# Kernel tuning notes

Measured on AMD Instinct MI355X. Metric: run time of the kernel, lower is better.

The kernel has to match this reference:

```python
import jax, jax.numpy as jnp
import numpy as np

N = 50000
E = 500000
D_IN = 128
D_HID = 128  # hidden_channels; conv1 outputs 2*D_HID


def setup_inputs() -> dict:
    key = jax.random.key(0)
    ks = jax.random.split(key, 8)
    x = jax.random.normal(ks[0], (N, D_IN), dtype=jnp.float32)
    edge_index = jax.random.randint(ks[1], (2, E), 0, N, dtype=jnp.int64)
    # Glorot-ish init for weights, zeros for biases (PyG GCNConv default style)
    W1 = jax.random.normal(ks[2], (D_IN, 2 * D_HID), dtype=jnp.float32) / np.sqrt(D_IN)
    b1 = jnp.zeros((2 * D_HID,), dtype=jnp.float32)
    W2 = jax.random.normal(ks[3], (2 * D_HID, D_HID), dtype=jnp.float32) / np.sqrt(2 * D_HID)
    b2 = jnp.zeros((D_HID,), dtype=jnp.float32)
    Wfc = jax.random.normal(ks[4], (D_HID, 6), dtype=jnp.float32) / np.sqrt(D_HID)
    bfc = jnp.zeros((6,), dtype=jnp.float32)
    return {"x": x, "W1": W1, "b1": b1, "W2": W2, "b2": b2,
            "Wfc": Wfc, "bfc": bfc, "edge_index": edge_index}


def _gcn_conv(x, W, b, src, dst, deg_isqrt, n):
    # PyG GCNConv: h = W x; out_i = sum_j norm_ij * h_j + b, with self-loops
    h = x @ W                                  # [n, d_out]
    norm = deg_isqrt[src] * deg_isqrt[dst]     # [E+n]
    msg = h[src] * norm[:, None]               # gather + scale
    out = jax.ops.segment_sum(msg, dst, num_segments=n)  # scatter-add
    return out + b


def reference(x, W1, b1, W2, b2, Wfc, bfc, edge_index):
    n = x.shape[0]
    loop = jnp.arange(n, dtype=edge_index.dtype)
    src = jnp.concatenate([edge_index[0], loop])  # add self-loops
    dst = jnp.concatenate([edge_index[1], loop])
    deg = jax.ops.segment_sum(jnp.ones_like(dst, dtype=x.dtype), dst, num_segments=n)
    deg_isqrt = jnp.where(deg > 0, jax.lax.rsqrt(jnp.maximum(deg, 1e-12)), 0.0)
    h = jax.nn.relu(_gcn_conv(x, W1, b1, src, dst, deg_isqrt, n))
    h = jax.nn.relu(_gcn_conv(h, W2, b2, src, dst, deg_isqrt, n))
    return h @ Wfc + bfc
```

## Files before the change

kernel.cpp:

```cpp
#include <hip/hip_runtime.h>


typedef _Float16 f16;
typedef __attribute__((ext_vector_type(8))) _Float16 f16x8;
typedef __attribute__((ext_vector_type(4))) float f32x4;

__global__ void count_kernel(const int* __restrict__ dst, int* __restrict__ cnt,
                             int e) {
    for (int i = blockIdx.x * blockDim.x + threadIdx.x; i < e;
         i += gridDim.x * blockDim.x)
        atomicAdd(&cnt[dst[i]], 1);
}

__global__ void scan1_kernel(const int* __restrict__ cnt, int* __restrict__ local,
                             int* __restrict__ partials, float* __restrict__ disq,
                             int n) {
    __shared__ int lds[256];
    int base = blockIdx.x * 1024;
    int t = threadIdx.x;
    int v[4];
    int sum = 0;
    #pragma unroll
    for (int j = 0; j < 4; j++) {
        int i = base + t * 4 + j;
        v[j] = (i < n) ? cnt[i] : 0;
        if (i < n) disq[i] = rsqrtf(1.0f + (float)v[j]);
        sum += v[j];
    }
    lds[t] = sum;
    __syncthreads();
    for (int off = 1; off < 256; off <<= 1) {
        int x = (t >= off) ? lds[t - off] : 0;
        __syncthreads();
        lds[t] += x;
        __syncthreads();
    }
    int excl = lds[t] - sum;
    if (t == 255) partials[blockIdx.x] = lds[255];
    int run = excl;
    #pragma unroll
    for (int j = 0; j < 4; j++) {
        int i = base + t * 4 + j;
        if (i < n) local[i] = run;
        run += v[j];
    }
}

__global__ void scan2_kernel(int* __restrict__ partials, int nb) {
    __shared__ int lds[1024];
    int t = threadIdx.x;
    int v = (t < nb) ? partials[t] : 0;
    lds[t] = v;
    __syncthreads();
    for (int off = 1; off < 1024; off <<= 1) {
        int x = (t >= off) ? lds[t - off] : 0;
        __syncthreads();
        lds[t] += x;
        __syncthreads();
    }
    if (t < nb) partials[t] = lds[t] - v;
}

__global__ void scan3_kernel(const int* __restrict__ local,
                             const int* __restrict__ partials,
                             int* __restrict__ row_ptr, int* __restrict__ cursor,
                             int n, int e_total) {
    int base = blockIdx.x * 1024;
    int add = partials[blockIdx.x];
    int t = threadIdx.x;
    #pragma unroll
    for (int j = 0; j < 4; j++) {
        int i = base + t * 4 + j;
        if (i < n) {
            int p = local[i] + add;
            row_ptr[i] = p;
            cursor[i] = p;
        }
    }
    if (blockIdx.x == 0 && t == 0) row_ptr[n] = e_total;
}

__global__ void csr_fill_kernel(const int* __restrict__ src, const int* __restrict__ dst,
                                int* __restrict__ cursor, int* __restrict__ esorted,
                                int e) {
    for (int i = blockIdx.x * blockDim.x + threadIdx.x; i < e;
         i += gridDim.x * blockDim.x) {
        int d = dst[i];
        int pos = atomicAdd(&cursor[d], 1);
        esorted[pos] = src[i];
    }
}

__global__ void scale_cvt_kernel(const float4* __restrict__ in,
                                 const float* __restrict__ disq,
                                 f16* __restrict__ out, long long n4) {
    long long i = blockIdx.x * (long long)blockDim.x + threadIdx.x;
    if (i >= n4) return;
    float4 v = in[i];
    float s = disq[i >> 5];
    union { f16 h[4]; short4 s4; } u;
    u.h[0] = (f16)(v.x * s); u.h[1] = (f16)(v.y * s);
    u.h[2] = (f16)(v.z * s); u.h[3] = (f16)(v.w * s);
    *(short4*)(out + i * 4) = u.s4;
}

__global__ void cvt_wt_kernel(const float* __restrict__ W, f16* __restrict__ Wt,
                              int K, int Nc) {
    int i = blockIdx.x * blockDim.x + threadIdx.x;
    if (i >= K * Nc) return;
    int n = i / K, k = i - n * K;
    Wt[i] = (f16)W[(long long)k * Nc + n];
}

template <int MODE>
__global__ __launch_bounds__(256)
void gemm_f16_kernel(const f16* __restrict__ A,
                     const f16* __restrict__ Bt,
                     f16* __restrict__ C,
                     const float* __restrict__ rowscale,
                     const float* __restrict__ bias,
                     int M, int K, int Nc) {
    __shared__ __align__(16) char smem[(128 * 64 + 64 * 64) * 2];
    char* As = smem;
    char* Bs = smem + 128 * 64 * 2;
    const int tid = threadIdx.x;
    const int lane = tid & 63;
    const int wid = tid >> 6;
    const int wr = wid >> 1;
    const int wc = wid & 1;
    const int row0 = blockIdx.y * 128;
    const int col0 = blockIdx.x * 64;

    f32x4 acc[4][2];
    #pragma unroll
    for (int mr = 0; mr < 4; mr++)
        #pragma unroll
        for (int nr = 0; nr < 2; nr++)
            acc[mr][nr] = (f32x4){0.f, 0.f, 0.f, 0.f};

    for (int k0 = 0; k0 < K; k0 += 64) {
        #pragma unroll
        for (int i = 0; i < 4; i++) {
            int flat = tid + i * 256;
            int r = flat >> 3, g = flat & 7;
            int gr = row0 + r;
            float4 v = {0.f, 0.f, 0.f, 0.f};
            if (gr < M) v = *(const float4*)(A + (long long)gr * K + k0 + g * 8);
            *(float4*)(As + r * 128 + ((g * 16) ^ ((r & 7) << 4))) = v;
        }
        #pragma unroll
        for (int i = 0; i < 2; i++) {
            int flat = tid + i * 256;
            int nn = flat >> 3, g = flat & 7;
            float4 v = *(const float4*)(Bt + (long long)(col0 + nn) * K + k0 + g * 8);
            *(float4*)(Bs + nn * 128 + ((g * 16) ^ ((nn & 7) << 4))) = v;
        }
        __syncthreads();
        #pragma unroll
        for (int ks = 0; ks < 2; ks++) {
            const int kb = (ks * 32 + ((lane >> 4) * 8)) * 2;
            f16x8 af[4], bf[2];
            #pragma unroll
            for (int mr = 0; mr < 4; mr++) {
                int r = wr * 64 + mr * 16 + (lane & 15);
                af[mr] = *(const f16x8*)(As + r * 128 + (kb ^ ((r & 7) << 4)));
            }
            #pragma unroll
            for (int nr = 0; nr < 2; nr++) {
                int c = wc * 32 + nr * 16 + (lane & 15);
                bf[nr] = *(const f16x8*)(Bs + c * 128 + (kb ^ ((c & 7) << 4)));
            }
            #pragma unroll
            for (int mr = 0; mr < 4; mr++)
                #pragma unroll
                for (int nr = 0; nr < 2; nr++)
                    acc[mr][nr] = __builtin_amdgcn_mfma_f32_16x16x32_f16(
                        af[mr], bf[nr], acc[mr][nr], 0, 0, 0);
        }
        __syncthreads();
    }
    float bv[2] = {0.f, 0.f};
    if (MODE == 1) {
        #pragma unroll
        for (int nr = 0; nr < 2; nr++)
            bv[nr] = bias[col0 + wc * 32 + nr * 16 + (lane & 15)];
    }
    #pragma unroll
    for (int mr = 0; mr < 4; mr++) {
        #pragma unroll
        for (int reg = 0; reg < 4; reg++) {
            int row = row0 + wr * 64 + mr * 16 + (lane >> 4) * 4 + reg;
            if (row < M) {
                float s = rowscale[row];
                int col = col0 + wc * 32 + (lane & 15);
                #pragma unroll
                for (int nr = 0; nr < 2; nr++) {
                    float v = acc[mr][nr][reg] * s;
                    if (MODE == 1) v = fmaxf(v + bv[nr], 0.0f);
                    C[(long long)row * Nc + col + nr * 16] = (f16)v;
                }
            }
        }
    }
}

__global__ void gather_sum_f16_kernel(const float4* __restrict__ h,
                                      float4* __restrict__ out,
                                      const int* __restrict__ row_ptr,
                                      const int* __restrict__ esorted,
                                      int n, int c8) {
    int lane = threadIdx.x & 63;
    long long wave = (blockIdx.x * (long long)blockDim.x + threadIdx.x) >> 6;
    int epw = 64 / c8;
    int sub = lane / c8;
    int sl = lane - sub * c8;
    long long node = wave * epw + sub;
    if (node >= n) return;
    int beg = row_ptr[node], end = row_ptr[node + 1];
    float acc[8];
    {
        float4 v = h[node * c8 + sl];
        const f16* hp = (const f16*)&v;
        #pragma unroll
        for (int j = 0; j < 8; j++) acc[j] = (float)hp[j];
    }
    for (int e = beg; e < end; e++) {
        int s = esorted[e];
        float4 v = h[(long long)s * c8 + sl];
        const f16* hp = (const f16*)&v;
        #pragma unroll
        for (int j = 0; j < 8; j++) acc[j] += (float)hp[j];
    }
    union { float4 f4; f16 hh[8]; } o;
    #pragma unroll
    for (int j = 0; j < 8; j++) o.hh[j] = (f16)acc[j];
    out[node * c8 + sl] = o.f4;
}

__global__ void gather_fc_kernel(const float4* __restrict__ t,
                                 const int* __restrict__ row_ptr,
                                 const int* __restrict__ esorted,
                                 const float* __restrict__ disq,
                                 const float* __restrict__ b2,
                                 const float* __restrict__ Wfc,
                                 const float* __restrict__ bfc,
                                 float* __restrict__ out, int n) {
    __shared__ float wf[6 * 132];
    for (int i = threadIdx.x; i < 6 * 128; i += 256) {
        int k = i >> 7, ch = i & 127;
        wf[k * 132 + ch] = Wfc[ch * 6 + k];
    }
    __syncthreads();
    int lane = threadIdx.x & 63;
    long long wave = (blockIdx.x * (long long)blockDim.x + threadIdx.x) >> 6;
    int sub = lane >> 4;
    int sl = lane & 15;
    long long node = wave * 4 + sub;
    if (node >= n) return;
    int beg = row_ptr[node], end = row_ptr[node + 1];
    float acc[8];
    {
        float4 v = t[node * 16 + sl];
        const f16* hp = (const f16*)&v;
        #pragma unroll
        for (int j = 0; j < 8; j++) acc[j] = (float)hp[j];
    }
    for (int e = beg; e < end; e++) {
        int s = esorted[e];
        float4 v = t[(long long)s * 16 + sl];
        const f16* hp = (const f16*)&v;
        #pragma unroll
        for (int j = 0; j < 8; j++) acc[j] += (float)hp[j];
    }
    float sc = disq[node];
    const float4* b4 = (const float4*)(b2 + sl * 8);
    float4 bb0 = b4[0], bb1 = b4[1];
    float bb[8] = {bb0.x, bb0.y, bb0.z, bb0.w, bb1.x, bb1.y, bb1.z, bb1.w};
    float h2[8];
    #pragma unroll
    for (int j = 0; j < 8; j++)
        h2[j] = fmaxf(fmaf(acc[j], sc, bb[j]), 0.0f);
    float p[6];
    #pragma unroll
    for (int k = 0; k < 6; k++) {
        float s = 0.f;
        #pragma unroll
        for (int j = 0; j < 8; j++) s += h2[j] * wf[k * 132 + sl * 8 + j];
        p[k] = s;
    }
    #pragma unroll
    for (int off = 8; off >= 1; off >>= 1)
        #pragma unroll
        for (int k = 0; k < 6; k++) p[k] += __shfl_down(p[k], off);
    if (sl == 0) {
        #pragma unroll
        for (int k = 0; k < 6; k++)
            out[(long long)node * 6 + k] = p[k] + bfc[k];
    }
}

extern "C" void kernel_launch(void* const* d_in, const int* in_sizes, int n_in,
                              void* d_out, int out_size, void* d_ws, size_t ws_size,
                              hipStream_t stream) {
    const float* x   = (const float*)d_in[0];
    const float* W1  = (const float*)d_in[1];
    const float* b1  = (const float*)d_in[2];
    const float* W2  = (const float*)d_in[3];
    const float* b2  = (const float*)d_in[4];
    const float* Wfc = (const float*)d_in[5];
    const float* bfc = (const float*)d_in[6];
    const int* edges = (const int*)d_in[7];

    const int N = in_sizes[0] / 128;
    const int E = in_sizes[7] / 2;
    const int* e_src = edges;
    const int* e_dst = edges + E;

    char* ws = (char*)d_ws;
    size_t off = 0;
    auto alloc = [&](size_t bytes) {
        void* p = ws + off;
        off += (bytes + 255) & ~(size_t)255;
        return p;
    };
    const int NB = (N + 1023) / 1024;
    float* disq     = (float*)alloc((size_t)N * 4);
    int*   cnt      = (int*)  alloc((size_t)N * 4);
    int*   slocal   = (int*)  alloc((size_t)N * 4);
    int*   partials = (int*)  alloc((size_t)NB * 4);
    int*   row_ptr  = (int*)  alloc((size_t)(N + 1) * 4);
    int*   cursor   = (int*)  alloc((size_t)N * 4);
    int*   esorted  = (int*)  alloc((size_t)E * 4);
    f16*   xs       = (f16*)  alloc((size_t)N * 128 * 2);
    f16*   wt1      = (f16*)  alloc((size_t)256 * 128 * 2);
    f16*   wt2      = (f16*)  alloc((size_t)128 * 256 * 2);
    f16*   agg1     = (f16*)  alloc((size_t)N * 128 * 2);
    f16*   h1       = (f16*)  alloc((size_t)N * 256 * 2);
    f16*   tbuf     = (f16*)  alloc((size_t)N * 128 * 2);
    (void)ws_size; (void)n_in;

    float* out = (float*)d_out; (void)out_size;

    hipMemsetAsync(cnt, 0, (size_t)N * sizeof(int), stream);
    count_kernel<<<2048, 256, 0, stream>>>(e_dst, cnt, E);
    scan1_kernel<<<NB, 256, 0, stream>>>(cnt, slocal, partials, disq, N);
    scan2_kernel<<<1, 1024, 0, stream>>>(partials, NB);
    scan3_kernel<<<NB, 256, 0, stream>>>(slocal, partials, row_ptr, cursor, N, E);
    csr_fill_kernel<<<2048, 256, 0, stream>>>(e_src, e_dst, cursor, esorted, E);

    {
        long long n4 = (long long)N * 128 / 4;
        scale_cvt_kernel<<<(int)((n4 + 255) / 256), 256, 0, stream>>>(
            (const float4*)x, disq, xs, n4);
    }
    cvt_wt_kernel<<<(128 * 256 + 255) / 256, 256, 0, stream>>>(W1, wt1, 128, 256);
    cvt_wt_kernel<<<(256 * 128 + 255) / 256, 256, 0, stream>>>(W2, wt2, 256, 128);

    {
        long long waves = ((long long)N + 3) / 4;
        int blocks = (int)((waves + 3) / 4);
        gather_sum_f16_kernel<<<blocks, 256, 0, stream>>>(
            (const float4*)xs, (float4*)agg1, row_ptr, esorted, N, 16);
    }
    {
        dim3 g(256 / 64, (N + 127) / 128);
        gemm_f16_kernel<1><<<g, 256, 0, stream>>>(agg1, wt1, h1, disq, b1,
                                                  N, 128, 256);
    }

    {
        dim3 g(128 / 64, (N + 127) / 128);
        gemm_f16_kernel<0><<<g, 256, 0, stream>>>(h1, wt2, tbuf, disq, nullptr,
                                                  N, 256, 128);
    }
    {
        long long waves = ((long long)N + 3) / 4;
        int blocks = (int)((waves + 3) / 4);
        gather_fc_kernel<<<blocks, 256, 0, stream>>>(
            (const float4*)tbuf, row_ptr, esorted, disq, b2, Wfc, bfc, out, N);
    }
}
```

Measured before the change: 240.2 us.

## Double-buffer GEMM with direct global-to-LDS loads, unroll gathers, merge convert kernels

The GEMM now double-buffers LDS tiles and uses global_load_lds to fetch A and B tiles directly into pre-swizzled shared memory, overlapping loads for the next K-tile with MFMA compute. Partial row tiles fall back to a register path. The two gather kernels unroll the neighbor loop by four so more independent loads are in flight, and the input and weight conversion kernels are merged into one launch. The aim is to hide memory latency and cut launch overhead, at the cost of doubled LDS usage per block, which may lower occupancy.

```diff
diff --git a/kernel.cpp b/kernel.cpp
--- a/kernel.cpp
+++ b/kernel.cpp
@@ -4,6 +4,11 @@
 typedef _Float16 f16;
 typedef __attribute__((ext_vector_type(8))) _Float16 f16x8;
 typedef __attribute__((ext_vector_type(4))) float f32x4;
+
+#define GLOAD16(g, l)                                                      \
+    __builtin_amdgcn_global_load_lds(                                      \
+        (const __attribute__((address_space(1))) void*)(g),                \
+        (__attribute__((address_space(3))) void*)(l), 16, 0, 0)
 
 __global__ void count_kernel(const int* __restrict__ dst, int* __restrict__ cnt,
                              int e) {
@@ -91,25 +96,33 @@
     }
 }
 
-__global__ void scale_cvt_kernel(const float4* __restrict__ in,
-                                 const float* __restrict__ disq,
-                                 f16* __restrict__ out, long long n4) {
+__global__ void cvt_all_kernel(const float4* __restrict__ x,
+                               const float* __restrict__ disq,
+                               f16* __restrict__ xs,
+                               const float* __restrict__ W1, f16* __restrict__ wt1,
+                               const float* __restrict__ W2, f16* __restrict__ wt2,
+                               long long n4) {
     long long i = blockIdx.x * (long long)blockDim.x + threadIdx.x;
-    if (i >= n4) return;
-    float4 v = in[i];
-    float s = disq[i >> 5];
-    union { f16 h[4]; short4 s4; } u;
-    u.h[0] = (f16)(v.x * s); u.h[1] = (f16)(v.y * s);
-    u.h[2] = (f16)(v.z * s); u.h[3] = (f16)(v.w * s);
-    *(short4*)(out + i * 4) = u.s4;
-}
-
-__global__ void cvt_wt_kernel(const float* __restrict__ W, f16* __restrict__ Wt,
-                              int K, int Nc) {
-    int i = blockIdx.x * blockDim.x + threadIdx.x;
-    if (i >= K * Nc) return;
-    int n = i / K, k = i - n * K;
-    Wt[i] = (f16)W[(long long)k * Nc + n];
+    if (i < n4) {
+        float4 v = x[i];
+        float s = disq[i >> 5];
+        union { f16 h[4]; short4 s4; } u;
+        u.h[0] = (f16)(v.x * s); u.h[1] = (f16)(v.y * s);
+        u.h[2] = (f16)(v.z * s); u.h[3] = (f16)(v.w * s);
+        *(short4*)(xs + i * 4) = u.s4;
+        return;
+    }
+    long long j = i - n4;
+    if (j < 32768) {
+        int nn = (int)(j >> 7), k = (int)(j & 127);
+        wt1[j] = (f16)W1[(long long)k * 256 + nn];
+        return;
+    }
+    j -= 32768;
+    if (j < 32768) {
+        int nn = (int)(j >> 8), k = (int)(j & 255);
+        wt2[j] = (f16)W2[(long long)k * 128 + nn];
+    }
 }
 
 template <int MODE>
@@ -120,9 +133,7 @@
                      const float* __restrict__ rowscale,
                      const float* __restrict__ bias,
                      int M, int K, int Nc) {
-    __shared__ __align__(16) char smem[(128 * 64 + 64 * 64) * 2];
-    char* As = smem;
-    char* Bs = smem + 128 * 64 * 2;
+    __shared__ __align__(16) char smem[2 * 24 * 1024];
     const int tid = threadIdx.x;
     const int lane = tid & 63;
     const int wid = tid >> 6;
@@ -130,6 +141,7 @@
     const int wc = wid & 1;
     const int row0 = blockIdx.y * 128;
     const int col0 = blockIdx.x * 64;
+    const bool rows_full = (row0 + 128 <= M);
 
     f32x4 acc[4][2];
     #pragma unroll
@@ -138,24 +150,43 @@
         for (int nr = 0; nr < 2; nr++)
             acc[mr][nr] = (f32x4){0.f, 0.f, 0.f, 0.f};
 
-    for (int k0 = 0; k0 < K; k0 += 64) {
-        #pragma unroll
-        for (int i = 0; i < 4; i++) {
-            int flat = tid + i * 256;
-            int r = flat >> 3, g = flat & 7;
-            int gr = row0 + r;
-            float4 v = {0.f, 0.f, 0.f, 0.f};
-            if (gr < M) v = *(const float4*)(A + (long long)gr * K + k0 + g * 8);
-            *(float4*)(As + r * 128 + ((g * 16) ^ ((r & 7) << 4))) = v;
+    auto stage = [&](int buf, int k0) {
+        char* as = smem + buf * (24 * 1024);
+        char* bs = as + 16 * 1024;
+        if (rows_full) {
+            #pragma unroll
+            for (int i = 0; i < 4; i++) {
+                int flat = i * 256 + tid;
+                int r = flat >> 3, gp = flat & 7;
+                int g = gp ^ (r & 7);
+                const f16* src = A + (long long)(row0 + r) * K + k0 + g * 8;
+                GLOAD16(src, as + (i * 256 + wid * 64) * 16);
+            }
+        } else {
+            #pragma unroll
+            for (int i = 0; i < 4; i++) {
+                int flat = i * 256 + tid;
+                int r = flat >> 3, gp = flat & 7;
+                int g = gp ^ (r & 7);
+                int gr = row0 + r;
+                float4 v = {0.f, 0.f, 0.f, 0.f};
+                if (gr < M) v = *(const float4*)(A + (long long)gr * K + k0 + g * 8);
+                *(float4*)(as + flat * 16) = v;
+            }
         }
         #pragma unroll
         for (int i = 0; i < 2; i++) {
-            int flat = tid + i * 256;
-            int nn = flat >> 3, g = flat & 7;
-            float4 v = *(const float4*)(Bt + (long long)(col0 + nn) * K + k0 + g * 8);
-            *(float4*)(Bs + nn * 128 + ((g * 16) ^ ((nn & 7) << 4))) = v;
+            int flat = i * 256 + tid;
+            int nn = flat >> 3, gp = flat & 7;
+            int g = gp ^ (nn & 7);
+            const f16* src = Bt + (long long)(col0 + nn) * K + k0 + g * 8;
+            GLOAD16(src, bs + (i * 256 + wid * 64) * 16);
         }
-        __syncthreads();
+    };
+
+    auto compute = [&](int buf) {
+        char* as = smem + buf * (24 * 1024);
+        char* bs = as + 16 * 1024;
         #pragma unroll
         for (int ks = 0; ks < 2; ks++) {
             const int kb = (ks * 32 + ((lane >> 4) * 8)) * 2;
@@ -163,12 +194,12 @@
             #pragma unroll
             for (int mr = 0; mr < 4; mr++) {
                 int r = wr * 64 + mr * 16 + (lane & 15);
-                af[mr] = *(const f16x8*)(As + r * 128 + (kb ^ ((r & 7) << 4)));
+                af[mr] = *(const f16x8*)(as + r * 128 + (kb ^ ((r & 7) << 4)));
             }
             #pragma unroll
             for (int nr = 0; nr < 2; nr++) {
                 int c = wc * 32 + nr * 16 + (lane & 15);
-                bf[nr] = *(const f16x8*)(Bs + c * 128 + (kb ^ ((c & 7) << 4)));
+                bf[nr] = *(const f16x8*)(bs + c * 128 + (kb ^ ((c & 7) << 4)));
             }
             #pragma unroll
             for (int mr = 0; mr < 4; mr++)
@@ -177,8 +208,19 @@
                     acc[mr][nr] = __builtin_amdgcn_mfma_f32_16x16x32_f16(
                         af[mr], bf[nr], acc[mr][nr], 0, 0, 0);
         }
+    };
+
+    const int nt = K >> 6;
+    stage(0, 0);
+    __syncthreads();
+    int cur = 0;
+    for (int t = 0; t < nt; t++) {
+        if (t + 1 < nt) stage(cur ^ 1, (t + 1) * 64);
+        compute(cur);
         __syncthreads();
-    }
+        cur ^= 1;
+    }
+
     float bv[2] = {0.f, 0.f};
     if (MODE == 1) {
         #pragma unroll
@@ -207,26 +249,38 @@
 __global__ void gather_sum_f16_kernel(const float4* __restrict__ h,
                                       float4* __restrict__ out,
                                       const int* __restrict__ row_ptr,
-                                      const int* __restrict__ esorted,
-                                      int n, int c8) {
+                                      const int* __restrict__ esorted, int n) {
     int lane = threadIdx.x & 63;
     long long wave = (blockIdx.x * (long long)blockDim.x + threadIdx.x) >> 6;
-    int epw = 64 / c8;
-    int sub = lane / c8;
-    int sl = lane - sub * c8;
-    long long node = wave * epw + sub;
+    int sub = lane >> 4;
+    int sl = lane & 15;
+    long long node = wave * 4 + sub;
     if (node >= n) return;
     int beg = row_ptr[node], end = row_ptr[node + 1];
     float acc[8];
     {
-        float4 v = h[node * c8 + sl];
+        float4 v = h[node * 16 + sl];
         const f16* hp = (const f16*)&v;
         #pragma unroll
         for (int j = 0; j < 8; j++) acc[j] = (float)hp[j];
     }
-    for (int e = beg; e < end; e++) {
+    int e = beg;
+    for (; e + 4 <= end; e += 4) {
+        int s0 = esorted[e], s1 = esorted[e + 1];
+        int s2 = esorted[e + 2], s3 = esorted[e + 3];
+        float4 v0 = h[(long long)s0 * 16 + sl];
+        float4 v1 = h[(long long)s1 * 16 + sl];
+        float4 v2 = h[(long long)s2 * 16 + sl];
+        float4 v3 = h[(long long)s3 * 16 + sl];
+        const f16 *p0 = (const f16*)&v0, *p1 = (const f16*)&v1;
+        const f16 *p2 = (const f16*)&v2, *p3 = (const f16*)&v3;
+        #pragma unroll
+        for (int j = 0; j < 8; j++)
+            acc[j] += (float)p0[j] + (float)p1[j] + (float)p2[j] + (float)p3[j];
+    }
+    for (; e < end; e++) {
         int s = esorted[e];
-        float4 v = h[(long long)s * c8 + sl];
+        float4 v = h[(long long)s * 16 + sl];
         const f16* hp = (const f16*)&v;
         #pragma unroll
         for (int j = 0; j < 8; j++) acc[j] += (float)hp[j];
@@ -234,7 +288,7 @@
     union { float4 f4; f16 hh[8]; } o;
     #pragma unroll
     for (int j = 0; j < 8; j++) o.hh[j] = (f16)acc[j];
-    out[node * c8 + sl] = o.f4;
+    out[node * 16 + sl] = o.f4;
 }
 
 __global__ void gather_fc_kernel(const float4* __restrict__ t,
@@ -265,7 +319,21 @@
         #pragma unroll
         for (int j = 0; j < 8; j++) acc[j] = (float)hp[j];
     }
-    for (int e = beg; e < end; e++) {
+    int e = beg;
+    for (; e + 4 <= end; e += 4) {
+        int s0 = esorted[e], s1 = esorted[e + 1];
+        int s2 = esorted[e + 2], s3 = esorted[e + 3];
+        float4 v0 = t[(long long)s0 * 16 + sl];
+        float4 v1 = t[(long long)s1 * 16 + sl];
+        float4 v2 = t[(long long)s2 * 16 + sl];
+        float4 v3 = t[(long long)s3 * 16 + sl];
+        const f16 *p0 = (const f16*)&v0, *p1 = (const f16*)&v1;
+        const f16 *p2 = (const f16*)&v2, *p3 = (const f16*)&v3;
+        #pragma unroll
+        for (int j = 0; j < 8; j++)
+            acc[j] += (float)p0[j] + (float)p1[j] + (float)p2[j] + (float)p3[j];
+    }
+    for (; e < end; e++) {
         int s = esorted[e];
         float4 v = t[(long long)s * 16 + sl];
         const f16* hp = (const f16*)&v;
@@ -350,17 +418,16 @@
 
     {
         long long n4 = (long long)N * 128 / 4;
-        scale_cvt_kernel<<<(int)((n4 + 255) / 256), 256, 0, stream>>>(
-            (const float4*)x, disq, xs, n4);
-    }
-    cvt_wt_kernel<<<(128 * 256 + 255) / 256, 256, 0, stream>>>(W1, wt1, 128, 256);
-    cvt_wt_kernel<<<(256 * 128 + 255) / 256, 256, 0, stream>>>(W2, wt2, 256, 128);
+        long long total = n4 + 32768 + 32768;
+        cvt_all_kernel<<<(int)((total + 255) / 256), 256, 0, stream>>>(
+            (const float4*)x, disq, xs, W1, wt1, W2, wt2, n4);
+    }
 
     {
         long long waves = ((long long)N + 3) / 4;
         int blocks = (int)((waves + 3) / 4);
         gather_sum_f16_kernel<<<blocks, 256, 0, stream>>>(
-            (const float4*)xs, (float4*)agg1, row_ptr, esorted, N, 16);
+            (const float4*)xs, (float4*)agg1, row_ptr, esorted, N);
     }
     {
         dim3 g(256 / 64, (N + 127) / 128);
```

Result: faster. 234.8 us (-2.2%).
